# Kernel optimization log

Hardware: AMD Instinct MI355X
Metric: run time of the kernel (lower is better)

## Reference

```python
import jax, jax.numpy as jnp
import numpy as np

D = 2048
H = 16
KV = 4
DH = D // H  # 128
REP = H // KV
ROPE_BASE = 10000.0


def _rope(x, pos):
    # x: (B, h, L, Dh), pos: (L,)
    half = x.shape[-1] // 2
    inv_freq = 1.0 / (ROPE_BASE ** (jnp.arange(0, half, dtype=jnp.float32) / half))
    ang = pos.astype(jnp.float32)[:, None] * inv_freq[None, :]          # (L, half)
    cos = jnp.concatenate([jnp.cos(ang), jnp.cos(ang)], axis=-1)        # (L, Dh)
    sin = jnp.concatenate([jnp.sin(ang), jnp.sin(ang)], axis=-1)
    x1, x2 = x[..., :half], x[..., half:]
    rot = jnp.concatenate([-x2, x1], axis=-1)
    return x * cos[None, None] + rot * sin[None, None]


def setup_inputs() -> dict:
    key = jax.random.key(0)
    ks = jax.random.split(key, 5)
    s = 1.0 / np.sqrt(D)
    return {
        "x": jax.random.normal(ks[0], (2, 2048, D), dtype=jnp.float32),
        "wq": jax.random.uniform(ks[1], (H * DH, D), jnp.float32, -s, s),
        "wk": jax.random.uniform(ks[2], (KV * DH, D), jnp.float32, -s, s),
        "wv": jax.random.uniform(ks[3], (KV * DH, D), jnp.float32, -s, s),
        "wo": jax.random.uniform(ks[4], (D, H * DH), jnp.float32, -s, s),
    }


def reference(x, wq, wk, wv, wo):
    B, T, _ = x.shape
    q = (x @ wq.T).reshape(B, T, H, DH).transpose(0, 2, 1, 3)    # (B,H,T,Dh)
    k = (x @ wk.T).reshape(B, T, KV, DH).transpose(0, 2, 1, 3)   # (B,KV,T,Dh)
    v = (x @ wv.T).reshape(B, T, KV, DH).transpose(0, 2, 1, 3)
    Tc = T  # no kv cache
    pos = jnp.arange(Tc)
    q = _rope(q, pos)
    k = _rope(k, pos)
    # GQA: repeat kv heads to match query heads
    k_full = jnp.repeat(k, REP, axis=1)                          # (B,H,Tc,Dh)
    v_full = jnp.repeat(v, REP, axis=1)
    scale = 1.0 / np.sqrt(DH)
    scores = jnp.einsum('bhtd,bhsd->bhts', q, k_full) * scale    # (B,H,T,Tc)
    row = jnp.arange(T)[:, None]
    col = jnp.arange(Tc)[None, :]
    causal = col <= row + (Tc - T)
    scores = jnp.where(causal[None, None], scores, -jnp.inf)
    attn = jax.nn.softmax(scores, axis=-1)
    out = jnp.einsum('bhts,bhsd->bhtd', attn, v_full)            # (B,H,T,Dh)
    out = out.transpose(0, 2, 1, 3).reshape(B, T, H * DH)
    return out @ wo.T
```

## Files before the change

kernel.cpp:

```cpp
#include <hip/hip_runtime.h>

typedef float f32x4 __attribute__((ext_vector_type(4)));
typedef short s16x8 __attribute__((ext_vector_type(8)));
typedef unsigned short u16;

__device__ __forceinline__ u16 f2bf(float f) {
    union { float f; unsigned u; } v; v.f = f;
    return (u16)((v.u + 0x7fffu + ((v.u >> 16) & 1u)) >> 16);
}
__device__ __forceinline__ float bf2f(u16 h) {
    union { unsigned u; float f; } v; v.u = ((unsigned)h) << 16;
    return v.f;
}
__device__ __forceinline__ float fast_exp2(float x) {
#if __has_builtin(__builtin_amdgcn_exp2f)
    return __builtin_amdgcn_exp2f(x);
#else
    return exp2f(x);
#endif
}

__device__ __forceinline__ void gload_lds16(const void* g, void* l) {
    __builtin_amdgcn_global_load_lds((__attribute__((address_space(1))) void*)g,
                                     (__attribute__((address_space(3))) void*)l, 16, 0, 0);
}

__global__ __launch_bounds__(256) void cvt_all(const float* __restrict__ x,  const float* __restrict__ wq,
                                               const float* __restrict__ wk, const float* __restrict__ wv,
                                               u16* __restrict__ xb, u16* __restrict__ wqkvb) {
    int u = blockIdx.x * 256 + threadIdx.x;
    const float* src;
    u16* dst;
    if (u < 1048576) { src = x + (size_t)u * 8; dst = xb + (size_t)u * 8; }
    else {
        int w = u - 1048576;
        dst = wqkvb + (size_t)w * 8;
        if (w < 524288)      src = wq + (size_t)w * 8;
        else if (w < 655360) src = wk + (size_t)(w - 524288) * 8;
        else                 src = wv + (size_t)(w - 655360) * 8;
    }
    const float4* p = (const float4*)src;
    float4 a = p[0], b = p[1];
    s16x8 o;
    o[0] = f2bf(a.x); o[1] = f2bf(a.y); o[2] = f2bf(a.z); o[3] = f2bf(a.w);
    o[4] = f2bf(b.x); o[5] = f2bf(b.y); o[6] = f2bf(b.z); o[7] = f2bf(b.w);
    *(s16x8*)dst = o;
}

__global__ __launch_bounds__(256) void cvt_kernel(const float* __restrict__ in,
                                                  u16* __restrict__ out, int n8) {
    int i = blockIdx.x * 256 + threadIdx.x;
    if (i >= n8) return;
    const float4* p = (const float4*)(in + (size_t)i * 8);
    float4 a = p[0], b = p[1];
    s16x8 o;
    o[0] = f2bf(a.x); o[1] = f2bf(a.y); o[2] = f2bf(a.z); o[3] = f2bf(a.w);
    o[4] = f2bf(b.x); o[5] = f2bf(b.y); o[6] = f2bf(b.z); o[7] = f2bf(b.w);
    *(s16x8*)(out + (size_t)i * 8) = o;
}

template<int OUT>
__global__ __launch_bounds__(256) void gemm128(const u16* __restrict__ A, const u16* __restrict__ B,
                                               void* __restrict__ C, void* __restrict__ Ck,
                                               void* __restrict__ Cv, int M, int N, int K) {
    __shared__ __align__(16) u16 Ald[128 * 64];
    __shared__ __align__(16) u16 Bld[128 * 64];
    const int t = threadIdx.x, wid = t >> 6, lane = t & 63;
    const int m0 = blockIdx.y * 128, n0 = blockIdx.x * 128;
    const int ml = lane & 15, quad = lane >> 4, m7 = ml & 7;
    const int wm = (wid & 1) * 64, wn = (wid >> 1) * 64;
    const int sr = lane >> 3, sc = lane & 7;

    f32x4 acc[4][4] = {};

    for (int k0 = 0; k0 < K; k0 += 64) {
        if (k0) __syncthreads();
        #pragma unroll
        for (int i = 0; i < 4; ++i) {
            int seg = wid * 4 + i;
            int r = seg * 8 + sr;
            int c = (sc ^ (r & 7)) * 8;
            gload_lds16(A + (size_t)(m0 + r) * K + k0 + c, &Ald[seg * 512]);
            gload_lds16(B + (size_t)(n0 + r) * K + k0 + c, &Bld[seg * 512]);
        }
        __syncthreads();
        #pragma unroll
        for (int kk = 0; kk < 64; kk += 32) {
            s16x8 af[4], bf[4];
            #pragma unroll
            for (int mi = 0; mi < 4; ++mi)
                af[mi] = *(const s16x8*)&Ald[(wm + mi * 16 + ml) * 64 + (((kk >> 3) + quad) ^ m7) * 8];
            #pragma unroll
            for (int ni = 0; ni < 4; ++ni)
                bf[ni] = *(const s16x8*)&Bld[(wn + ni * 16 + ml) * 64 + (((kk >> 3) + quad) ^ m7) * 8];
            #pragma unroll
            for (int mi = 0; mi < 4; ++mi)
                #pragma unroll
                for (int ni = 0; ni < 4; ++ni)
                    acc[mi][ni] = __builtin_amdgcn_mfma_f32_16x16x32_bf16(af[mi], bf[ni], acc[mi][ni], 0, 0, 0);
        }
    }
    #pragma unroll
    for (int mi = 0; mi < 4; ++mi)
        #pragma unroll
        for (int ni = 0; ni < 4; ++ni) {
            int gmb = m0 + wm + mi * 16 + quad * 4;
            int gn  = n0 + wn + ni * 16 + ml;
            if constexpr (OUT == 4) {
                if (n0 < 2048) {
                    #pragma unroll
                    for (int r = 0; r < 4; ++r)
                        ((u16*)C)[(size_t)(gmb + r) * 2048 + gn] = f2bf(acc[mi][ni][r]);
                } else if (n0 < 2560) {
                    #pragma unroll
                    for (int r = 0; r < 4; ++r)
                        ((u16*)Ck)[(size_t)(gmb + r) * 512 + (gn - 2048)] = f2bf(acc[mi][ni][r]);
                } else {
                    ushort4 v;
                    v.x = f2bf(acc[mi][ni][0]); v.y = f2bf(acc[mi][ni][1]);
                    v.z = f2bf(acc[mi][ni][2]); v.w = f2bf(acc[mi][ni][3]);
                    *(ushort4*)((u16*)Cv + (size_t)(gn - 2560) * M + gmb) = v;
                }
            } else {
                #pragma unroll
                for (int r = 0; r < 4; ++r)
                    ((float*)C)[(size_t)(gmb + r) * N + gn] = acc[mi][ni][r];
            }
        }
}

__global__ __launch_bounds__(256) void rope_kernel(u16* __restrict__ qb, u16* __restrict__ kb,
                                                   int nq, int ntot, float sq) {
    int idx = blockIdx.x * 256 + threadIdx.x;
    if (idx >= ntot) return;
    u16* base; int nheads; float scl; int id;
    if (idx < nq) { base = qb; nheads = 16; scl = sq;  id = idx; }
    else          { base = kb; nheads = 4;  scl = 1.f; id = idx - nq; }
    int i = id & 63;
    int rest = id >> 6;
    int hh = rest % nheads;
    int tok = rest / nheads;
    int tpos = tok & 2047;
    u16* row = base + (size_t)tok * nheads * 128 + hh * 128;
    float x1 = bf2f(row[i]);
    float x2 = bf2f(row[i + 64]);
    float inv = expf(-(float)i * 0.14391156731570787f);
    float ang = (float)tpos * inv;
    float s, c;
    sincosf(ang, &s, &c);
    row[i]      = f2bf((x1 * c - x2 * s) * scl);
    row[i + 64] = f2bf((x2 * c + x1 * s) * scl);
}

__global__ __launch_bounds__(256, 4) void attn_kernel(const u16* __restrict__ Q, const u16* __restrict__ Kb,
                                                      const u16* __restrict__ Vt, u16* __restrict__ O) {
    __shared__ __align__(16) u16 Klds[64 * 128];
    __shared__ __align__(16) u16 Vlds[128 * 64];
    __shared__ __align__(16) u16 Plds[4][16 * 64];
    const int t = threadIdx.x, wslot = t >> 6, lane = t & 63;
    const int kv = blockIdx.y, b = blockIdx.z;
    const int g = kv + 4 * b;
    const int bx = blockIdx.x;
    int qt;
    switch ((g >> 1) & 3) {
        case 0:  qt = bx; break;
        case 1:  qt = 127 - bx; break;
        case 2:  qt = (bx + 64) & 127; break;
        default: qt = (63 - bx) & 127; break;
    }
    const int h = kv * 4 + wslot;
    const int ml = lane & 15, quad = lane >> 4, m7 = ml & 7;
    const int t0 = qt * 16;
    const int n = (qt >> 2) + 1;

    s16x8 qf[4];
    {
        const u16* qp = Q + ((size_t)(b * 2048 + t0 + ml) * 2048 + h * 128);
        #pragma unroll
        for (int kc = 0; kc < 4; ++kc)
            qf[kc] = *(const s16x8*)(qp + kc * 32 + quad * 8);
    }

    s16x8 ones;
    #pragma unroll
    for (int j = 0; j < 8; ++j) ones[j] = (short)0x3F80;

    f32x4 Oa[8] = {};
    f32x4 L = {};

    for (int it = 0; it < n; ++it) {
        const int s0 = it * 64;
        if (it) __syncthreads();
        #pragma unroll
        for (int i = 0; i < 4; ++i) {
            int seg = wslot * 4 + i;
            int kr = seg * 4 + (lane >> 4);
            int kc = ((lane & 15) ^ (kr & 7)) * 8;
            gload_lds16(Kb + (size_t)(b * 2048 + s0 + kr) * 512 + kv * 128 + kc, &Klds[seg * 512]);
            int vr = seg * 8 + (lane >> 3);
            int vc = ((lane & 7) ^ (vr & 7)) * 8;
            gload_lds16(Vt + (size_t)(kv * 128 + vr) * 4096 + b * 2048 + s0 + vc, &Vlds[seg * 512]);
        }
        __syncthreads();

        f32x4 S[4] = {};
        #pragma unroll
        for (int kc = 0; kc < 4; ++kc)
            #pragma unroll
            for (int ti = 0; ti < 4; ++ti) {
                s16x8 kf = *(const s16x8*)&Klds[(ti * 16 + ml) * 128 + ((kc * 4 + quad) ^ m7) * 8];
                S[ti] = __builtin_amdgcn_mfma_f32_16x16x32_bf16(qf[kc], kf, S[ti], 0, 0, 0);
            }

        {
            u16* pl = &Plds[wslot][0];
            const bool diag = (it == n - 1);
            #pragma unroll
            for (int r = 0; r < 4; ++r) {
                int qr = t0 + quad * 4 + r;
                int row = quad * 4 + r;
                #pragma unroll
                for (int ti = 0; ti < 4; ++ti) {
                    float e = fast_exp2(S[ti][r]);
                    if (diag && (s0 + ti * 16 + ml > qr)) e = 0.f;
                    union { float f; unsigned u; } cv; cv.f = e;
                    pl[row * 64 + (((ti * 2 + (ml >> 3)) ^ (row & 7)) * 8) + (ml & 7)] = (u16)(cv.u >> 16);
                }
            }
        }
        asm volatile("s_waitcnt lgkmcnt(0)" ::: "memory");
        s16x8 pf[2];
        pf[0] = *(const s16x8*)&Plds[wslot][ml * 64 + ((quad)     ^ m7) * 8];
        pf[1] = *(const s16x8*)&Plds[wslot][ml * 64 + ((4 + quad) ^ m7) * 8];
        asm volatile("s_waitcnt lgkmcnt(0)" ::: "memory");

        #pragma unroll
        for (int c = 0; c < 2; ++c) {
            #pragma unroll
            for (int nt = 0; nt < 8; ++nt) {
                s16x8 vf = *(const s16x8*)&Vlds[(nt * 16 + ml) * 64 + ((c * 4 + quad) ^ m7) * 8];
                Oa[nt] = __builtin_amdgcn_mfma_f32_16x16x32_bf16(pf[c], vf, Oa[nt], 0, 0, 0);
            }
            L = __builtin_amdgcn_mfma_f32_16x16x32_bf16(pf[c], ones, L, 0, 0, 0);
        }
    }

    #pragma unroll
    for (int nt = 0; nt < 8; ++nt)
        #pragma unroll
        for (int r = 0; r < 4; ++r) {
            int col = h * 128 + nt * 16 + ml;
            O[(size_t)(b * 2048 + t0 + quad * 4 + r) * 2048 + col] = f2bf(Oa[nt][r] / L[r]);
        }
}

extern "C" void kernel_launch(void* const* d_in, const int* in_sizes, int n_in,
                              void* d_out, int out_size, void* d_ws, size_t ws_size,
                              hipStream_t stream) {
    const float* x  = (const float*)d_in[0];
    const float* wq = (const float*)d_in[1];
    const float* wk = (const float*)d_in[2];
    const float* wv = (const float*)d_in[3];
    const float* wo = (const float*)d_in[4];
    float* out = (float*)d_out;
    char* ws = (char*)d_ws;

    const size_t MB = 1024 * 1024;
    u16* xb    = (u16*)(ws);
    u16* qb    = (u16*)(ws + 16 * MB);
    u16* kb    = (u16*)(ws + 32 * MB);
    u16* vtb   = (u16*)(ws + 36 * MB);
    u16* wqkvb = (u16*)(ws + 40 * MB);
    u16* ab    = xb;
    u16* wob   = wqkvb;

    cvt_all<<<7168, 256, 0, stream>>>(x, wq, wk, wv, xb, wqkvb);

    gemm128<4><<<dim3(24, 32), 256, 0, stream>>>(xb, wqkvb, qb, kb, vtb, 4096, 3072, 2048);

    cvt_kernel<<<2048, 256, 0, stream>>>(wo, wob, 524288);

    rope_kernel<<<20480, 256, 0, stream>>>(qb, kb, 4194304, 5242880, 0.12751743f);

    attn_kernel<<<dim3(128, 4, 2), 256, 0, stream>>>(qb, kb, vtb, ab);

    gemm128<1><<<dim3(16, 32), 256, 0, stream>>>(ab, wob, out, nullptr, nullptr, 4096, 2048, 2048);
}
```

Measured before the change: 334.6 us.

## Split long causal attention rows across two blocks with atomic accumulation

Adds a split-KV attention path. Query tiles in the second half of the sequence, which have the most causal work, have their KV range split between two workgroups, and tiles are ordered longest-first to balance load across CUs. The partial unnormalized outputs and row sums are combined with float atomicAdd into a zeroed fp32 workspace, then a separate kernel normalizes and converts them to bf16. This is intended to cut the tail imbalance of the causal workload, at the cost of two extra launches, atomic traffic and an fp32 scratch buffer. The path only runs when the workspace is at least 70 MB.

```diff
diff --git a/kernel.cpp b/kernel.cpp
--- a/kernel.cpp
+++ b/kernel.cpp
@@ -57,6 +57,31 @@
     o[0] = f2bf(a.x); o[1] = f2bf(a.y); o[2] = f2bf(a.z); o[3] = f2bf(a.w);
     o[4] = f2bf(b.x); o[5] = f2bf(b.y); o[6] = f2bf(b.z); o[7] = f2bf(b.w);
     *(s16x8*)(out + (size_t)i * 8) = o;
+}
+
+__global__ __launch_bounds__(256) void zero_acc(float* __restrict__ p, int n4) {
+    int i = blockIdx.x * 256 + threadIdx.x;
+    if (i >= n4) return;
+    float4 z = {0.f, 0.f, 0.f, 0.f};
+    ((float4*)p)[i] = z;
+}
+
+__global__ __launch_bounds__(256) void norm_split(const float* __restrict__ Oacc,
+                                                  const float* __restrict__ Lacc,
+                                                  u16* __restrict__ ab) {
+    int i = blockIdx.x * 256 + threadIdx.x;
+    int rowi = i >> 8;
+    int col0 = (i & 255) * 8;
+    const float* po = Oacc + ((size_t)rowi << 11) + col0;
+    float Lv = Lacc[rowi * 16 + (col0 >> 7)];
+    float inv = 1.0f / Lv;
+    int b = rowi >> 10, tokp = rowi & 1023;
+    u16* pd = ab + ((size_t)(b * 2048 + 1024 + tokp) << 11) + col0;
+    float4 a = ((const float4*)po)[0], c = ((const float4*)po)[1];
+    s16x8 o;
+    o[0] = f2bf(a.x * inv); o[1] = f2bf(a.y * inv); o[2] = f2bf(a.z * inv); o[3] = f2bf(a.w * inv);
+    o[4] = f2bf(c.x * inv); o[5] = f2bf(c.y * inv); o[6] = f2bf(c.z * inv); o[7] = f2bf(c.w * inv);
+    *(s16x8*)pd = o;
 }
 
 template<int OUT>
@@ -254,6 +279,136 @@
         }
 }
 
+__global__ __launch_bounds__(256, 4) void attn_split(const u16* __restrict__ Q, const u16* __restrict__ Kb,
+                                                     const u16* __restrict__ Vt, u16* __restrict__ O,
+                                                     float* __restrict__ Oacc, float* __restrict__ Lacc) {
+    __shared__ __align__(16) u16 Klds[64 * 128];
+    __shared__ __align__(16) u16 Vlds[128 * 64];
+    __shared__ __align__(16) u16 Plds[4][16 * 64];
+    const int t = threadIdx.x, wslot = t >> 6, lane = t & 63;
+    const int id = blockIdx.x;
+    const int g = id & 7, w = id >> 3;
+    const int kv = g & 3, b = g >> 2;
+
+    int qt, it0, it1, nfull;
+    bool partial;
+    if (w < 128) {
+        qt = 127 - (w >> 1);
+        nfull = (qt >> 2) + 1;
+        int nA = nfull >> 1;
+        if ((w & 1) == 0) { it0 = 0;  it1 = nA; }
+        else              { it0 = nA; it1 = nfull; }
+        partial = true;
+    } else {
+        qt = 191 - w;
+        nfull = (qt >> 2) + 1;
+        it0 = 0; it1 = nfull;
+        partial = false;
+    }
+
+    const int h = kv * 4 + wslot;
+    const int ml = lane & 15, quad = lane >> 4, m7 = ml & 7;
+    const int t0 = qt * 16;
+
+    s16x8 qf[4];
+    {
+        const u16* qp = Q + ((size_t)(b * 2048 + t0 + ml) * 2048 + h * 128);
+        #pragma unroll
+        for (int kc = 0; kc < 4; ++kc)
+            qf[kc] = *(const s16x8*)(qp + kc * 32 + quad * 8);
+    }
+
+    s16x8 ones;
+    #pragma unroll
+    for (int j = 0; j < 8; ++j) ones[j] = (short)0x3F80;
+
+    f32x4 Oa[8] = {};
+    f32x4 L = {};
+
+    for (int it = it0; it < it1; ++it) {
+        const int s0 = it * 64;
+        if (it != it0) __syncthreads();
+        #pragma unroll
+        for (int i = 0; i < 4; ++i) {
+            int seg = wslot * 4 + i;
+            int kr = seg * 4 + (lane >> 4);
+            int kc = ((lane & 15) ^ (kr & 7)) * 8;
+            gload_lds16(Kb + (size_t)(b * 2048 + s0 + kr) * 512 + kv * 128 + kc, &Klds[seg * 512]);
+            int vr = seg * 8 + (lane >> 3);
+            int vc = ((lane & 7) ^ (vr & 7)) * 8;
+            gload_lds16(Vt + (size_t)(kv * 128 + vr) * 4096 + b * 2048 + s0 + vc, &Vlds[seg * 512]);
+        }
+        __syncthreads();
+
+        f32x4 S[4] = {};
+        #pragma unroll
+        for (int kc = 0; kc < 4; ++kc)
+            #pragma unroll
+            for (int ti = 0; ti < 4; ++ti) {
+                s16x8 kf = *(const s16x8*)&Klds[(ti * 16 + ml) * 128 + ((kc * 4 + quad) ^ m7) * 8];
+                S[ti] = __builtin_amdgcn_mfma_f32_16x16x32_bf16(qf[kc], kf, S[ti], 0, 0, 0);
+            }
+
+        {
+            u16* pl = &Plds[wslot][0];
+            const bool diag = (it == nfull - 1);
+            #pragma unroll
+            for (int r = 0; r < 4; ++r) {
+                int qr = t0 + quad * 4 + r;
+                int row = quad * 4 + r;
+                #pragma unroll
+                for (int ti = 0; ti < 4; ++ti) {
+                    float e = fast_exp2(S[ti][r]);
+                    if (diag && (s0 + ti * 16 + ml > qr)) e = 0.f;
+                    union { float f; unsigned u; } cv; cv.f = e;
+                    pl[row * 64 + (((ti * 2 + (ml >> 3)) ^ (row & 7)) * 8) + (ml & 7)] = (u16)(cv.u >> 16);
+                }
+            }
+        }
+        asm volatile("s_waitcnt lgkmcnt(0)" ::: "memory");
+        s16x8 pf[2];
+        pf[0] = *(const s16x8*)&Plds[wslot][ml * 64 + ((quad)     ^ m7) * 8];
+        pf[1] = *(const s16x8*)&Plds[wslot][ml * 64 + ((4 + quad) ^ m7) * 8];
+        asm volatile("s_waitcnt lgkmcnt(0)" ::: "memory");
+
+        #pragma unroll
+        for (int c = 0; c < 2; ++c) {
+            #pragma unroll
+            for (int nt = 0; nt < 8; ++nt) {
+                s16x8 vf = *(const s16x8*)&Vlds[(nt * 16 + ml) * 64 + ((c * 4 + quad) ^ m7) * 8];
+                Oa[nt] = __builtin_amdgcn_mfma_f32_16x16x32_bf16(pf[c], vf, Oa[nt], 0, 0, 0);
+            }
+            L = __builtin_amdgcn_mfma_f32_16x16x32_bf16(pf[c], ones, L, 0, 0, 0);
+        }
+    }
+
+    if (!partial) {
+        #pragma unroll
+        for (int nt = 0; nt < 8; ++nt)
+            #pragma unroll
+            for (int r = 0; r < 4; ++r) {
+                int col = h * 128 + nt * 16 + ml;
+                O[(size_t)(b * 2048 + t0 + quad * 4 + r) * 2048 + col] = f2bf(Oa[nt][r] / L[r]);
+            }
+    } else {
+        const int tokp = (qt - 64) * 16;
+        #pragma unroll
+        for (int nt = 0; nt < 8; ++nt)
+            #pragma unroll
+            for (int r = 0; r < 4; ++r) {
+                size_t row = (size_t)(b * 1024 + tokp + quad * 4 + r);
+                atomicAdd(&Oacc[row * 2048 + h * 128 + nt * 16 + ml], Oa[nt][r]);
+            }
+        if (ml == 0) {
+            #pragma unroll
+            for (int r = 0; r < 4; ++r) {
+                size_t row = (size_t)(b * 1024 + tokp + quad * 4 + r);
+                atomicAdd(&Lacc[row * 16 + h], L[r]);
+            }
+        }
+    }
+}
+
 extern "C" void kernel_launch(void* const* d_in, const int* in_sizes, int n_in,
                               void* d_out, int out_size, void* d_ws, size_t ws_size,
                               hipStream_t stream) {
@@ -274,6 +429,8 @@
     u16* ab    = xb;
     u16* wob   = wqkvb;
 
+    const bool split = ws_size >= 70 * MB;
+
     cvt_all<<<7168, 256, 0, stream>>>(x, wq, wk, wv, xb, wqkvb);
 
     gemm128<4><<<dim3(24, 32), 256, 0, stream>>>(xb, wqkvb, qb, kb, vtb, 4096, 3072, 2048);
@@ -282,7 +439,15 @@
 
     rope_kernel<<<20480, 256, 0, stream>>>(qb, kb, 4194304, 5242880, 0.12751743f);
 
-    attn_kernel<<<dim3(128, 4, 2), 256, 0, stream>>>(qb, kb, vtb, ab);
+    if (split) {
+        float* Oacc = (float*)(ws + 52 * MB);
+        float* Lacc = (float*)(ws + 68 * MB);
+        zero_acc<<<4128, 256, 0, stream>>>(Oacc, 1056768);
+        attn_split<<<1536, 256, 0, stream>>>(qb, kb, vtb, ab, Oacc, Lacc);
+        norm_split<<<2048, 256, 0, stream>>>(Oacc, Lacc, ab);
+    } else {
+        attn_kernel<<<dim3(128, 4, 2), 256, 0, stream>>>(qb, kb, vtb, ab);
+    }
 
     gemm128<1><<<dim3(16, 32), 256, 0, stream>>>(ab, wob, out, nullptr, nullptr, 4096, 2048, 2048);
 }
```

Result: slower. 342.3 us (+2.3%).
